# Performance work log

Measured on AMD Instinct MI355X. Metric: run time of the kernel, lower is better.

Reference implementation:

```python
import jax, jax.numpy as jnp
import numpy as np

B, H, N, D = 2, 8, 2048, 64


def setup_inputs() -> dict:
    key = jax.random.key(0)
    kq, kk, kv = jax.random.split(key, 3)
    q = jax.random.normal(kq, (B, H, N, D), dtype=jnp.float32)
    k = jax.random.normal(kk, (B, H, N, D), dtype=jnp.float32)
    v = jax.random.normal(kv, (B, H, N, D), dtype=jnp.float32)
    return {"q": q, "k": k, "v": v}


def _selective_attn(sim):
    # sim: (b, h, i, j). Gate computed from first head, relu'd, SOS unmasked,
    # diagonal zeroed, shifted down one row, cumsum over query rows, subtracted.
    b, h, i, j = sim.shape
    gate = jax.nn.relu(sim[:, 0])                       # (b, i, j)
    gate = gate.at[:, :, j - i].set(0.0)                # no_mask_sos: column -i
    eye = jnp.eye(i, dtype=sim.dtype)
    if j > i:
        eye = jnp.pad(eye, ((0, 0), (j - i, 0)), constant_values=1.0)
    gate = (1.0 - eye) * gate
    # F.pad(gate, (0,0,1,-1)): shift rows down by one, drop last row
    gate = jnp.pad(gate, ((0, 0), (1, 0), (0, 0)))[:, :i, :]
    gate = jnp.cumsum(gate, axis=-2)
    return sim - gate[:, None]                          # broadcast over heads


def reference(q, k, v):
    scale = q.shape[-1] ** -0.5
    i, j = q.shape[-2], k.shape[-2]

    # squared L2 distance scores: ||q||^2 + ||k||^2 - 2 q.k  (== cdist(q,k)**2)
    q_sq = jnp.sum(q * q, axis=-1)                      # (b, h, i)
    k_sq = jnp.sum(k * k, axis=-1)                      # (b, h, j)
    qk = jnp.einsum('bhid,bhjd->bhij', q, k)            # (b, h, i, j)
    d2 = jnp.maximum(q_sq[..., :, None] + k_sq[..., None, :] - 2.0 * qk, 0.0)
    sim = -d2 * scale

    # causal mask (triu with offset j - i + 1)
    mask_value = -jnp.finfo(sim.dtype).max
    causal = jnp.triu(jnp.ones((i, j), dtype=bool), j - i + 1)
    sim = jnp.where(causal, mask_value, sim)

    # selective attention gating
    sim = _selective_attn(sim)

    # one-hot straight-through attention
    idx = jnp.argmax(sim, axis=-1)                      # (b, h, i)
    hard = jax.nn.one_hot(idx, j, dtype=sim.dtype)      # (b, h, i, j)
    soft = jax.nn.softmax(sim, axis=-1)
    attn = hard + soft - jax.lax.stop_gradient(soft)

    return jnp.einsum('bhij,bhjd->bhid', attn, v)
```

## Files before the change

### kernel.cpp

```cpp
#include <hip/hip_runtime.h>
#include <stdint.h>

#define B_ 2
#define H_ 8
#define N_ 2048
#define D_ 64
#define BH_ (B_ * H_)
#define NROWS (BH_ * N_)
#define TPB_ 272
#define TASKS (TPB_ * BH_)
#define EPSF 8e-3f
#define INFF __int_as_float(0x7f800000)

using u64 = unsigned long long;
using u32 = unsigned int;
typedef __attribute__((ext_vector_type(8))) short short8;
typedef __attribute__((ext_vector_type(4))) float f32x4;

#define MFMA16(A, B, C) __builtin_amdgcn_mfma_f32_16x16x32_bf16((A), (B), (C), 0, 0, 0)

__global__ __launch_bounds__(256) void prep_k(
    const float* __restrict__ k, char* __restrict__ khi_g,
    char* __restrict__ klo_g, float* __restrict__ ksq_g,
    u32* __restrict__ count)
{
  if (blockIdx.x == 0 && threadIdx.x == 0) count[0] = 0;
  const int t = (int)blockIdx.x * 256 + threadIdx.x;
  const int r = t >> 3, kg = t & 7;
  const float* kp = k + (size_t)r * D_ + kg * 8;
  const float4 f0 = *(const float4*)kp;
  const float4 f1 = *(const float4*)(kp + 4);
  const float vv[8] = {f0.x, f0.y, f0.z, f0.w, f1.x, f1.y, f1.z, f1.w};
  u32 hw[4], lw[4];
  float ps = 0.f;
  #pragma unroll
  for (int e = 0; e < 4; ++e) {
    const float va = vv[2 * e], vb = vv[2 * e + 1];
    ps = fmaf(va, va, ps); ps = fmaf(vb, vb, ps);
    const u32 ha = __float_as_uint(va) & 0xFFFF0000u;
    const u32 hb = __float_as_uint(vb) & 0xFFFF0000u;
    hw[e] = (ha >> 16) | hb;
    const u32 la = __float_as_uint(va - __uint_as_float(ha));
    const u32 lb = __float_as_uint(vb - __uint_as_float(hb));
    lw[e] = (la >> 16) | (lb & 0xFFFF0000u);
  }
  const size_t off = ((size_t)(r >> 4) * 2 + (kg >> 2)) * 1024 +
                     (size_t)(((kg & 3) << 4) + (r & 15)) * 16;
  *(uint4*)(khi_g + off) = make_uint4(hw[0], hw[1], hw[2], hw[3]);
  *(uint4*)(klo_g + off) = make_uint4(lw[0], lw[1], lw[2], lw[3]);
  float ssum = ps;
  ssum += __shfl_xor(ssum, 1);
  ssum += __shfl_xor(ssum, 2);
  ssum += __shfl_xor(ssum, 4);
  if (kg == 0) ksq_g[r] = ssum;
}

__device__ __forceinline__ void cvt_hilo(const float* p, short8& hi, short8& lo) {
  const float4 f0 = *(const float4*)p;
  const float4 f1 = *(const float4*)(p + 4);
  const float vv[8] = {f0.x, f0.y, f0.z, f0.w, f1.x, f1.y, f1.z, f1.w};
  #pragma unroll
  for (int e = 0; e < 8; ++e) {
    const float v = vv[e];
    const u32 hb = __float_as_uint(v) & 0xFFFF0000u;
    hi[e] = (short)(hb >> 16);
    lo[e] = (short)(__float_as_uint(v - __uint_as_float(hb)) >> 16);
  }
}

__global__ __launch_bounds__(64, 3) void phase1(
    const float* __restrict__ q, const char* __restrict__ khi_g,
    const char* __restrict__ klo_g, const float* __restrict__ ksq_g,
    u64* __restrict__ bestc, u32* __restrict__ secc)
{
  const int b = (int)blockIdx.x;
  const int task = (b & 7) * (TASKS / 8) + (b >> 3);
  const int bh = task / TPB_;
  const int rem = task - bh * TPB_;
  int t = 0;
  while ((t + 1) * (t + 2) <= rem) ++t;
  const int idx = rem - t * (t + 1);
  const int qn = idx / (t + 1);
  const int g4 = 2 * t + qn;
  const int c = idx - qn * (t + 1);
  const int jfirst = c * 8;
  const int jlast = min(jfirst + 7, 4 * g4 + 3);

  const int lane = threadIdx.x & 63;
  const int grp = lane >> 4, c0 = lane & 15;
  const int i0 = g4 * 64;

  short8 ah[4][2], al[4][2];
  #pragma unroll
  for (int s = 0; s < 4; ++s) {
    const float* qrow =
        q + ((size_t)bh * N_ + i0 + s * 16 + c0) * D_ + grp * 8;
    cvt_hilo(qrow, ah[s][0], al[s][0]);
    cvt_hilo(qrow + 32, ah[s][1], al[s][1]);
  }

  float bf[4][4], sf[4][4];
  u32 bj[4][4];
  #pragma unroll
  for (int s = 0; s < 4; ++s)
    #pragma unroll
    for (int r2 = 0; r2 < 4; ++r2) {
      bf[s][r2] = INFF; sf[s][r2] = INFF; bj[s][r2] = 0;
    }

  const size_t fb = (size_t)bh * 128 * 2048;
  const char* ph = khi_g + fb + (size_t)jfirst * 2048 + lane * 16;
  const char* pl = klo_g + fb + (size_t)jfirst * 2048 + lane * 16;
  const float* pk = ksq_g + (size_t)bh * N_ + jfirst * 16 + c0;

  short8 ch0 = *(const short8*)(ph);
  short8 ch1 = *(const short8*)(ph + 1024);
  short8 cl0 = *(const short8*)(pl);
  short8 cl1 = *(const short8*)(pl + 1024);
  float cks = *pk;

  for (int js = jfirst; js <= jlast; ++js) {
    const int adv = (js < jlast) ? 1 : 0;
    const short8 nh0 = *(const short8*)(ph + adv * 2048);
    const short8 nh1 = *(const short8*)(ph + adv * 2048 + 1024);
    const short8 nl0 = *(const short8*)(pl + adv * 2048);
    const short8 nl1 = *(const short8*)(pl + adv * 2048 + 1024);
    const float nks = pk[adv * 16];
    ph += adv * 2048; pl += adv * 2048; pk += adv * 16;

    const int jcol = js * 16 + c0;
    #pragma unroll
    for (int s = 0; s < 4; ++s) {
      if (js > 4 * g4 + s) continue;
      const bool dsub = (js == 4 * g4 + s);
      f32x4 aA = {0.f, 0.f, 0.f, 0.f}, aB = {0.f, 0.f, 0.f, 0.f};
      aA = MFMA16(ah[s][0], ch0, aA);  aB = MFMA16(ah[s][1], ch1, aB);
      aA = MFMA16(ah[s][0], cl0, aA);  aB = MFMA16(ah[s][1], cl1, aB);
      aA = MFMA16(al[s][0], ch0, aA);  aB = MFMA16(al[s][1], ch1, aB);
      #pragma unroll
      for (int reg = 0; reg < 4; ++reg) {
        float score = fmaf(-2.f, aA[reg] + aB[reg], cks);
        if (dsub && jcol > i0 + s * 16 + grp * 4 + reg) score = INFF;
        const float loser = fmaxf(bf[s][reg], score);
        sf[s][reg] = fminf(sf[s][reg], loser);
        if (score < bf[s][reg]) bj[s][reg] = (u32)jcol;
        bf[s][reg] = fminf(bf[s][reg], score);
      }
    }
    ch0 = nh0; ch1 = nh1; cl0 = nl0; cl1 = nl1; cks = nks;
  }

  #pragma unroll
  for (int s = 0; s < 4; ++s) {
    #pragma unroll
    for (int reg = 0; reg < 4; ++reg) {
      const u32 bbits = __float_as_uint(bf[s][reg]);
      const u32 key = bbits ^ (u32)(((int)bbits >> 31) | 0x80000000);
      u64 pkk = ((u64)key << 32) | bj[s][reg];
      float sv = sf[s][reg];
      #pragma unroll
      for (int m = 1; m < 16; m <<= 1) {
        const u64 opk = (u64)__shfl_xor((long long)pkk, m);
        const float osv = __shfl_xor(sv, m);
        const u32 mk = (u32)(pkk >> 32), ok = (u32)(opk >> 32);
        const u32 lk = (opk < pkk) ? mk : ok;
        const u32 lb = (lk & 0x80000000u) ? (lk ^ 0x80000000u) : ~lk;
        sv = fminf(fminf(sv, osv), __uint_as_float(lb));
        if (opk < pkk) pkk = opk;
      }
      if (c0 == 0) {
        const size_t rr = (size_t)bh * N_ + i0 + s * 16 + grp * 4 + reg;
        bestc[(size_t)c * NROWS + rr] = pkk;
        secc[(size_t)c * NROWS + rr] = __float_as_uint(sv);
      }
    }
  }
}

__global__ __launch_bounds__(256) void combine_gather(
    const u64* __restrict__ bestc, const u32* __restrict__ secc,
    const float* __restrict__ v, float* __restrict__ out,
    u32* __restrict__ flaglist, u32* __restrict__ count)
{
  __shared__ u64 pk_s[4][64];
  __shared__ float s1_s[4][64];
  __shared__ u32 idx_s[64];
  const int tid = threadIdx.x;
  const int r0 = (int)blockIdx.x * 64;
  const int p = tid >> 6, t6 = tid & 63;

  {
    const int r = r0 + t6;
    const int i = r & (N_ - 1);
    const int nch = ((i >> 6) + 2) >> 1;
    u64 b0 = ~0ull;
    float bcur = INFF, s1 = INFF;
    int cstar = -1;
    for (int c2 = p; c2 < nch; c2 += 4) {
      const u64 kk = bestc[(size_t)c2 * NROWS + r];
      const u32 key = (u32)(kk >> 32);
      const u32 bits = (key & 0x80000000u) ? (key ^ 0x80000000u) : ~key;
      const float f = __uint_as_float(bits);
      if (kk < b0) { s1 = fminf(s1, bcur); b0 = kk; bcur = f; cstar = c2; }
      else s1 = fminf(s1, f);
    }
    if (cstar >= 0)
      s1 = fminf(s1, __uint_as_float(secc[(size_t)cstar * NROWS + r]));
    pk_s[p][t6] = b0;
    s1_s[p][t6] = s1;
  }
  __syncthreads();

  if (tid < 64) {
    u64 b0 = ~0ull;
    float bcur = INFF, s1 = INFF;
    #pragma unroll
    for (int pp = 0; pp < 4; ++pp) {
      const u64 kk = pk_s[pp][tid];
      const u32 key = (u32)(kk >> 32);
      const u32 bits = (key & 0x80000000u) ? (key ^ 0x80000000u) : ~key;
      const float f = __uint_as_float(bits);
      if (kk < b0) { s1 = fminf(s1, bcur); b0 = kk; bcur = f; }
      else s1 = fminf(s1, f);
      s1 = fminf(s1, s1_s[pp][tid]);
    }
    idx_s[tid] = (u32)(b0 & 0xFFFFu);
    if ((s1 - bcur) < EPSF) {
      const u32 pos = atomicAdd(count, 1u);
      flaglist[pos] = (u32)(r0 + tid);
    }
  }
  __syncthreads();

  #pragma unroll
  for (int iter = 0; iter < 4; ++iter) {
    const int tk = tid + iter * 256;
    const int rl = tk >> 4, cc = tk & 15;
    const int r = r0 + rl;
    const u32 j = idx_s[rl];
    const int bh = r >> 11;
    const float4 val = ((const float4*)(v + ((size_t)bh * N_ + j) * D_))[cc];
    ((float4*)(out + (size_t)r * D_))[cc] = val;
  }
}

__global__ __launch_bounds__(64) void exact_partial(
    const float* __restrict__ q, const float* __restrict__ k,
    const u32* __restrict__ flaglist, const u32* __restrict__ count,
    double* __restrict__ pd, int* __restrict__ pj)
{
  const int lane = threadIdx.x & 63;
  const int cnt = (int)count[0];
  for (int t = blockIdx.x; (t >> 4) < cnt; t += (int)gridDim.x) {
    const int li = t >> 4, slice = t & 15;
    const int r = (int)flaglist[li];
    const int bh = r >> 11;
    const int i = r & (N_ - 1);
    const int jbase = slice * 128;

    double bbest = 1e300;
    int bjj = 0x7FFFFFFF;
    if (jbase <= i) {
      const float4* qr = (const float4*)(q + (size_t)r * D_);
      float4 qv[16];
      #pragma unroll
      for (int t2 = 0; t2 < 16; ++t2) qv[t2] = qr[t2];
      double s0 = 0, s1 = 0, s2 = 0, s3 = 0;
      #pragma unroll
      for (int t2 = 0; t2 < 16; ++t2) {
        s0 = fma((double)qv[t2].x, (double)qv[t2].x, s0);
        s1 = fma((double)qv[t2].y, (double)qv[t2].y, s1);
        s2 = fma((double)qv[t2].z, (double)qv[t2].z, s2);
        s3 = fma((double)qv[t2].w, (double)qv[t2].w, s3);
      }
      const double qsqd = (s0 + s1) + (s2 + s3);
      const float* kb = k + (size_t)bh * N_ * D_;

      #pragma unroll
      for (int u = 0; u < 2; ++u) {
        const int j = jbase + u * 64 + lane;
        if (j <= i) {
          const float4* kr = (const float4*)(kb + (size_t)j * D_);
          double a0 = 0, a1 = 0, a2 = 0, a3 = 0;
          double t0 = 0, t1 = 0, t2d = 0, t3 = 0;
          #pragma unroll
          for (int t2 = 0; t2 < 16; ++t2) {
            const float4 kv = kr[t2];
            const double k0 = kv.x, k1 = kv.y, k2 = kv.z, k3 = kv.w;
            a0 = fma((double)qv[t2].x, k0, a0);
            a1 = fma((double)qv[t2].y, k1, a1);
            a2 = fma((double)qv[t2].z, k2, a2);
            a3 = fma((double)qv[t2].w, k3, a3);
            t0 = fma(k0, k0, t0);
            t1 = fma(k1, k1, t1);
            t2d = fma(k2, k2, t2d);
            t3 = fma(k3, k3, t3);
          }
          const double raw = (qsqd + ((t0 + t1) + (t2d + t3))) -
                             2.0 * ((a0 + a1) + (a2 + a3));
          const double d2 = raw > 0.0 ? raw : 0.0;
          if (d2 < bbest) { bbest = d2; bjj = j; }
        }
      }
      #pragma unroll
      for (int m = 1; m < 64; m <<= 1) {
        const double ob = __shfl_xor(bbest, m);
        const int oj = __shfl_xor(bjj, m);
        if (ob < bbest || (ob == bbest && oj < bjj)) { bbest = ob; bjj = oj; }
      }
    }
    if (lane == 0) {
      pd[(size_t)li * 16 + slice] = bbest;
      pj[(size_t)li * 16 + slice] = bjj;
    }
  }
}

__global__ __launch_bounds__(64) void exact_final(
    const double* __restrict__ pd, const int* __restrict__ pj,
    const u32* __restrict__ flaglist, const u32* __restrict__ count,
    const float* __restrict__ v, float* __restrict__ out)
{
  const int lane = threadIdx.x & 63;
  const int cnt = (int)count[0];
  for (int li = blockIdx.x; li < cnt; li += (int)gridDim.x) {
    const int r = (int)flaglist[li];
    const int bh = r >> 11;
    double d = (lane < 16) ? pd[(size_t)li * 16 + lane] : 1e300;
    int j = (lane < 16) ? pj[(size_t)li * 16 + lane] : 0x7FFFFFFF;
    #pragma unroll
    for (int m = 1; m < 16; m <<= 1) {
      const double od = __shfl_xor(d, m);
      const int oj = __shfl_xor(j, m);
      if (od < d || (od == d && oj < j)) { d = od; j = oj; }
    }
    if (lane < 16) {
      const float4 val =
          ((const float4*)(v + ((size_t)bh * N_ + j) * D_))[lane];
      ((float4*)(out + (size_t)r * D_))[lane] = val;
    }
  }
}

extern "C" void kernel_launch(void* const* d_in, const int* in_sizes, int n_in,
                              void* d_out, int out_size, void* d_ws,
                              size_t ws_size, hipStream_t stream) {
  const float* q = (const float*)d_in[0];
  const float* k = (const float*)d_in[1];
  const float* v = (const float*)d_in[2];
  float* out = (float*)d_out;

  char* ws = (char*)d_ws;
  u32* count = (u32*)ws;
  u32* flaglist = (u32*)(ws + 4096);
  float* ksq_g = (float*)(ws + 256 * 1024);
  char* khi_g = ws + 1ull * 1024 * 1024;
  char* klo_g = ws + 8ull * 1024 * 1024;
  u64* bestc = (u64*)(ws + 16ull * 1024 * 1024);
  u32* secc = (u32*)(ws + 24ull * 1024 * 1024);
  double* pd = (double*)(ws + 32ull * 1024 * 1024);
  int* pj = (int*)(ws + 40ull * 1024 * 1024);

  prep_k<<<(NROWS * 8) / 256, 256, 0, stream>>>(k, khi_g, klo_g, ksq_g, count);
  phase1<<<TASKS, 64, 0, stream>>>(q, khi_g, klo_g, ksq_g, bestc, secc);
  combine_gather<<<NROWS / 64, 256, 0, stream>>>(bestc, secc, v, out,
                                                 flaglist, count);
  exact_partial<<<2048, 64, 0, stream>>>(q, k, flaglist, count, pd, pj);
  exact_final<<<256, 64, 0, stream>>>(pd, pj, flaglist, count, v, out);
}
```

Before: 62.82 us.

## Halve phase1 query tile to 32 rows and double-buffer K loads two steps ahead

The phase1 work decomposition changes from 64-row query groups to 32-row groups. This doubles the task count and reduces per-wave accumulator state from 4 to 2 subtiles. The K-column loop now processes two 16-column steps per iteration and prefetches the next two, deepening the load pipeline. The occupancy hint drops from 3 to 2 waves because the extra prefetch registers are needed. Smaller tiles mean less reuse of each K load and more partial results to combine, and combine_gather's chunk count formula is updated to match.

Result: faster. 56.54 us (-10.0%).

```diff
diff --git a/kernel.cpp b/kernel.cpp
--- a/kernel.cpp
+++ b/kernel.cpp
@@ -7,7 +7,7 @@
 #define D_ 64
 #define BH_ (B_ * H_)
 #define NROWS (BH_ * N_)
-#define TPB_ 272
+#define TPB_ 544
 #define TASKS (TPB_ * BH_)
 #define EPSF 8e-3f
 #define INFF __int_as_float(0x7f800000)
@@ -68,7 +68,7 @@
   }
 }
 
-__global__ __launch_bounds__(64, 3) void phase1(
+__global__ __launch_bounds__(64, 2) void phase1(
     const float* __restrict__ q, const char* __restrict__ khi_g,
     const char* __restrict__ klo_g, const float* __restrict__ ksq_g,
     u64* __restrict__ bestc, u32* __restrict__ secc)
@@ -77,69 +77,67 @@
   const int task = (b & 7) * (TASKS / 8) + (b >> 3);
   const int bh = task / TPB_;
   const int rem = task - bh * TPB_;
-  int t = 0;
-  while ((t + 1) * (t + 2) <= rem) ++t;
-  const int idx = rem - t * (t + 1);
-  const int qn = idx / (t + 1);
-  const int g4 = 2 * t + qn;
-  const int c = idx - qn * (t + 1);
+  int a = 0;
+  while (2 * (a + 1) * (a + 2) <= rem) ++a;
+  const int idx = rem - 2 * a * (a + 1);
+  const int g2 = 4 * a + idx / (a + 1);
+  const int c = idx - (idx / (a + 1)) * (a + 1);
   const int jfirst = c * 8;
-  const int jlast = min(jfirst + 7, 4 * g4 + 3);
+  const int jlast = min(jfirst + 7, 2 * g2 + 1);
 
   const int lane = threadIdx.x & 63;
   const int grp = lane >> 4, c0 = lane & 15;
-  const int i0 = g4 * 64;
-
-  short8 ah[4][2], al[4][2];
-  #pragma unroll
-  for (int s = 0; s < 4; ++s) {
+  const int i0 = g2 * 32;
+
+  const size_t fb = (size_t)bh * 128 * 2048;
+  const char* ph = khi_g + fb + (size_t)jfirst * 2048 + lane * 16;
+  const char* pl = klo_g + fb + (size_t)jfirst * 2048 + lane * 16;
+  const float* pk = ksq_g + (size_t)bh * N_ + jfirst * 16 + c0;
+
+  const int a1 = (jfirst < jlast) ? 1 : 0;
+  short8 S0h0 = *(const short8*)(ph);
+  short8 S0h1 = *(const short8*)(ph + 1024);
+  short8 S0l0 = *(const short8*)(pl);
+  short8 S0l1 = *(const short8*)(pl + 1024);
+  float  S0k  = pk[0];
+  short8 S1h0 = *(const short8*)(ph + a1 * 2048);
+  short8 S1h1 = *(const short8*)(ph + a1 * 2048 + 1024);
+  short8 S1l0 = *(const short8*)(pl + a1 * 2048);
+  short8 S1l1 = *(const short8*)(pl + a1 * 2048 + 1024);
+  float  S1k  = pk[a1 * 16];
+
+  short8 ah[2][2], al[2][2];
+  #pragma unroll
+  for (int s = 0; s < 2; ++s) {
     const float* qrow =
         q + ((size_t)bh * N_ + i0 + s * 16 + c0) * D_ + grp * 8;
     cvt_hilo(qrow, ah[s][0], al[s][0]);
     cvt_hilo(qrow + 32, ah[s][1], al[s][1]);
   }
 
-  float bf[4][4], sf[4][4];
-  u32 bj[4][4];
-  #pragma unroll
-  for (int s = 0; s < 4; ++s)
+  float bf[2][4], sf[2][4];
+  u32 bj[2][4];
+  #pragma unroll
+  for (int s = 0; s < 2; ++s)
     #pragma unroll
     for (int r2 = 0; r2 < 4; ++r2) {
       bf[s][r2] = INFF; sf[s][r2] = INFF; bj[s][r2] = 0;
     }
 
-  const size_t fb = (size_t)bh * 128 * 2048;
-  const char* ph = khi_g + fb + (size_t)jfirst * 2048 + lane * 16;
-  const char* pl = klo_g + fb + (size_t)jfirst * 2048 + lane * 16;
-  const float* pk = ksq_g + (size_t)bh * N_ + jfirst * 16 + c0;
-
-  short8 ch0 = *(const short8*)(ph);
-  short8 ch1 = *(const short8*)(ph + 1024);
-  short8 cl0 = *(const short8*)(pl);
-  short8 cl1 = *(const short8*)(pl + 1024);
-  float cks = *pk;
-
-  for (int js = jfirst; js <= jlast; ++js) {
-    const int adv = (js < jlast) ? 1 : 0;
-    const short8 nh0 = *(const short8*)(ph + adv * 2048);
-    const short8 nh1 = *(const short8*)(ph + adv * 2048 + 1024);
-    const short8 nl0 = *(const short8*)(pl + adv * 2048);
-    const short8 nl1 = *(const short8*)(pl + adv * 2048 + 1024);
-    const float nks = pk[adv * 16];
-    ph += adv * 2048; pl += adv * 2048; pk += adv * 16;
-
+  auto compute = [&](int js, const short8& h0, const short8& h1,
+                     const short8& l0, const short8& l1, float ks) {
     const int jcol = js * 16 + c0;
     #pragma unroll
-    for (int s = 0; s < 4; ++s) {
-      if (js > 4 * g4 + s) continue;
-      const bool dsub = (js == 4 * g4 + s);
+    for (int s = 0; s < 2; ++s) {
+      if (js > 2 * g2 + s) continue;
+      const bool dsub = (js == 2 * g2 + s);
       f32x4 aA = {0.f, 0.f, 0.f, 0.f}, aB = {0.f, 0.f, 0.f, 0.f};
-      aA = MFMA16(ah[s][0], ch0, aA);  aB = MFMA16(ah[s][1], ch1, aB);
-      aA = MFMA16(ah[s][0], cl0, aA);  aB = MFMA16(ah[s][1], cl1, aB);
-      aA = MFMA16(al[s][0], ch0, aA);  aB = MFMA16(al[s][1], ch1, aB);
+      aA = MFMA16(ah[s][0], h0, aA);  aB = MFMA16(ah[s][1], h1, aB);
+      aA = MFMA16(ah[s][0], l0, aA);  aB = MFMA16(ah[s][1], l1, aB);
+      aA = MFMA16(al[s][0], h0, aA);  aB = MFMA16(al[s][1], h1, aB);
       #pragma unroll
       for (int reg = 0; reg < 4; ++reg) {
-        float score = fmaf(-2.f, aA[reg] + aB[reg], cks);
+        float score = fmaf(-2.f, aA[reg] + aB[reg], ks);
         if (dsub && jcol > i0 + s * 16 + grp * 4 + reg) score = INFF;
         const float loser = fmaxf(bf[s][reg], score);
         sf[s][reg] = fminf(sf[s][reg], loser);
@@ -147,11 +145,35 @@
         bf[s][reg] = fminf(bf[s][reg], score);
       }
     }
-    ch0 = nh0; ch1 = nh1; cl0 = nl0; cl1 = nl1; cks = nks;
-  }
-
-  #pragma unroll
-  for (int s = 0; s < 4; ++s) {
+  };
+
+  int js = jfirst;
+  for (; js + 1 <= jlast; js += 2) {
+    const int a2 = min(2, jlast - js);
+    const int a3 = min(3, jlast - js);
+    short8 N0h0 = *(const short8*)(ph + a2 * 2048);
+    short8 N0h1 = *(const short8*)(ph + a2 * 2048 + 1024);
+    short8 N0l0 = *(const short8*)(pl + a2 * 2048);
+    short8 N0l1 = *(const short8*)(pl + a2 * 2048 + 1024);
+    float  N0k  = pk[a2 * 16];
+    short8 N1h0 = *(const short8*)(ph + a3 * 2048);
+    short8 N1h1 = *(const short8*)(ph + a3 * 2048 + 1024);
+    short8 N1l0 = *(const short8*)(pl + a3 * 2048);
+    short8 N1l1 = *(const short8*)(pl + a3 * 2048 + 1024);
+    float  N1k  = pk[a3 * 16];
+
+    compute(js,     S0h0, S0h1, S0l0, S0l1, S0k);
+    compute(js + 1, S1h0, S1h1, S1l0, S1l1, S1k);
+
+    S0h0 = N0h0; S0h1 = N0h1; S0l0 = N0l0; S0l1 = N0l1; S0k = N0k;
+    S1h0 = N1h0; S1h1 = N1h1; S1l0 = N1l0; S1l1 = N1l1; S1k = N1k;
+    ph += 2 * 2048; pl += 2 * 2048; pk += 32;
+  }
+  if (js <= jlast)
+    compute(js, S0h0, S0h1, S0l0, S0l1, S0k);
+
+  #pragma unroll
+  for (int s = 0; s < 2; ++s) {
     #pragma unroll
     for (int reg = 0; reg < 4; ++reg) {
       const u32 bbits = __float_as_uint(bf[s][reg]);
@@ -192,7 +214,7 @@
   {
     const int r = r0 + t6;
     const int i = r & (N_ - 1);
-    const int nch = ((i >> 6) + 2) >> 1;
+    const int nch = (2 * (i >> 5) + 9) >> 3;
     u64 b0 = ~0ull;
     float bcur = INFF, s1 = INFF;
     int cstar = -1;
```
